# Kernel tuning notes

Hardware: AMD Instinct MI355X
Metric: run time of the kernel (lower is better)

The kernel has to match this reference:

```python
import jax, jax.numpy as jnp
from jax import lax
import numpy as np

SHIFT = 0.0
BN_EPS = 1e-5
THRESHOLD = 0.9
GAMMA = 1.0


def _maxpool2(x):
    # 2x2 max pool, stride 2, NCHW
    return lax.reduce_window(x, -jnp.inf, lax.max, (1, 1, 2, 2), (1, 1, 2, 2), 'VALID')


def _conv(x, w, b):
    y = lax.conv_general_dilated(x, w, (1, 1), 'SAME',
                                 dimension_numbers=('NCHW', 'OIHW', 'NCHW'))
    return y + b[None, :, None, None]


def setup_inputs() -> dict:
    key = jax.random.key(0)
    ks = jax.random.split(key, 12)
    B = 8192
    x = jax.random.normal(ks[0], (B, 1, 28, 28), dtype=jnp.float32)
    conv1_w = jax.random.normal(ks[1], (8, 1, 3, 3), dtype=jnp.float32) * 0.1
    conv1_b = jax.random.normal(ks[2], (8,), dtype=jnp.float32) * 0.1
    conv2_w = jax.random.normal(ks[3], (16, 8, 3, 3), dtype=jnp.float32) * 0.1
    conv2_b = jax.random.normal(ks[4], (16,), dtype=jnp.float32) * 0.1
    fc1_w = jax.random.normal(ks[5], (64, 784), dtype=jnp.float32) * 0.05
    fc1_b = jax.random.normal(ks[6], (64,), dtype=jnp.float32) * 0.05
    fc2_w = jax.random.normal(ks[7], (4, 64), dtype=jnp.float32) * 0.1
    fc2_b = jax.random.normal(ks[8], (4,), dtype=jnp.float32) * 0.1
    bn_gamma = jnp.ones((4,), dtype=jnp.float32)
    bn_beta = jnp.zeros((4,), dtype=jnp.float32)
    return dict(x=x, conv1_w=conv1_w, conv1_b=conv1_b, conv2_w=conv2_w,
                conv2_b=conv2_b, fc1_w=fc1_w, fc1_b=fc1_b, fc2_w=fc2_w,
                fc2_b=fc2_b, bn_gamma=bn_gamma, bn_beta=bn_beta)


def reference(x, conv1_w, conv1_b, conv2_w, conv2_b, fc1_w, fc1_b,
              fc2_w, fc2_b, bn_gamma, bn_beta):
    B = x.shape[0]
    # CNN feature extractor
    h = _maxpool2(jax.nn.relu(_conv(x, conv1_w, conv1_b)))   # [B,8,14,14]
    h = _maxpool2(jax.nn.relu(_conv(h, conv2_w, conv2_b)))   # [B,16,7,7]
    flat = h.reshape(B, -1)                                   # [B,784]
    h = jax.nn.relu(flat @ fc1_w.T + fc1_b)                   # [B,64]
    proj = h @ fc2_w.T + fc2_b                                # [B,4]
    # BatchNorm1d (training mode: batch stats, biased variance)
    mean = jnp.mean(proj, axis=0)
    var = jnp.mean((proj - mean) ** 2, axis=0)
    proj = (proj - mean) * lax.rsqrt(var + BN_EPS) * bn_gamma + bn_beta
    # fidelity adjacency (vectorized O(B^2) pairwise squared cosine overlap)
    pn = proj / (jnp.linalg.norm(proj, axis=1, keepdims=True) + 1e-12)
    fid = (pn @ pn.T) ** 2                                    # [B,B]
    off_diag = 1.0 - jnp.eye(B, dtype=proj.dtype)
    adj = jnp.where(fid >= THRESHOLD, 1.0, 0.0) * off_diag
    adj = lax.stop_gradient(adj)  # built via .item() in torch -> detached
    weighted_proj = adj @ proj                                # [B,4]
    # RBF kernel over the fully-flattened feature matrices (scalar)
    diff = proj - weighted_proj
    k_val = jnp.exp(-GAMMA * jnp.sum(diff * diff))
    # combined.sum(dim=1) == row sums + scalar kernel value
    logits = (jnp.sum(proj, axis=1, keepdims=True)
              + jnp.sum(weighted_proj, axis=1, keepdims=True)
              + k_val)                                        # [B,1]
    probs = jax.nn.sigmoid(logits + SHIFT)
    return jnp.concatenate([probs, 1.0 - probs], axis=-1)     # [B,2]
```

## Files before the change

kernel.cpp:

```cpp
#include <hip/hip_runtime.h>
#include <hip/hip_bf16.h>

#define B_IMG 8192
#define FC_ROWS 8
#define FC_NBLK (B_IMG / FC_ROWS)

#define OFF_SD    64
#define OFF_PROJ  128
#define OFF_PN64  (128 + 262144)
#define OFF_PB32  (OFF_PN64 + 262144)
#define OFF_PN32  (OFF_PB32 + 131072)
#define OFF_WP32  (OFF_PN32 + 131072)
#define OFF_W1T   (OFF_WP32 + 131072)
#define OFF_PSUM  (OFF_W1T + 200704)
#define OFF_FLAT  1310720
#define FLAT64_BYTES (8192UL * 784UL * 8UL)

#define H1_CS   10
#define H1_RP   164

__global__ __launch_bounds__(256) void setup_kernel(
    const float* __restrict__ fc1w, float* __restrict__ w1t,
    float* __restrict__ sd) {
    const int t = threadIdx.x;
    if (blockIdx.x == 0 && t == 0) sd[0] = 0.f;
    for (int i = blockIdx.x * 256 + t; i < 784 * 64; i += 64 * 256) {
        const int o = i & 63, k = i >> 6;
        w1t[i] = fc1w[o * 784 + k];
    }
}

template <int BUF>
__device__ __forceinline__ void ldpair(
    double2 (&W)[2][4][2][2], const double* __restrict__ h1s,
    int rowb, int c0, int icp) {
#pragma unroll
    for (int wr = 0; wr < 4; ++wr) {
#pragma unroll
        for (int cc = 0; cc < 2; ++cc) {
            const double* p = h1s + (rowb + wr) * H1_RP + (c0 + cc) * H1_CS + icp * 4;
            W[BUF][wr][cc][0] = *(const double2*)p;
            W[BUF][wr][cc][1] = *(const double2*)(p + 2);
        }
    }
}

template <int PHASE>
__device__ __forceinline__ void conv2_step(
    const double2 (&W)[2][4][2][2], const double (&wgt)[9][4],
    double bias2, int c2, int icp, int pys, int px,
    double* __restrict__ h2s) {
    double s00 = 0, s01 = 0, s10 = 0, s11 = 0;
#pragma unroll
    for (int dy = 0; dy < 2; ++dy)
#pragma unroll
        for (int dx = 0; dx < 2; ++dx)
#pragma unroll
            for (int ky = 0; ky < 3; ++ky)
#pragma unroll
                for (int kx = 0; kx < 3; ++kx) {
                    const int wr = dy + ky, wc = dx + kx;
                    const int buf = (wc < 2) ? PHASE : (1 - PHASE);
                    const int sl = wc & 1;
                    double2 lo = W[buf][wr][sl][0];
                    double2 hi = W[buf][wr][sl][1];
                    double a = (dy == 0) ? ((dx == 0) ? s00 : s01)
                                         : ((dx == 0) ? s10 : s11);
                    a = fma(lo.x, wgt[ky * 3 + kx][0], a);
                    a = fma(lo.y, wgt[ky * 3 + kx][1], a);
                    a = fma(hi.x, wgt[ky * 3 + kx][2], a);
                    a = fma(hi.y, wgt[ky * 3 + kx][3], a);
                    if (dy == 0) { if (dx == 0) s00 = a; else s01 = a; }
                    else         { if (dx == 0) s10 = a; else s11 = a; }
                }
    s00 += __shfl_xor(s00, 16);
    s01 += __shfl_xor(s01, 16);
    s10 += __shfl_xor(s10, 16);
    s11 += __shfl_xor(s11, 16);
    if (icp == 0) {
        double mx = fmax(fmax(s00, s01), fmax(s10, s11));
        h2s[c2 * 49 + pys * 7 + px] = fmax(bias2 + mx, 0.0);
    }
}

template <bool F64OUT>
__global__ __launch_bounds__(256) void conv_fused(
    const float* __restrict__ x,
    const float* __restrict__ w1, const float* __restrict__ b1,
    const float* __restrict__ w2, const float* __restrict__ b2,
    void* __restrict__ flatv) {

    __shared__ __align__(16) float  xs[900];
    __shared__ __align__(16) double h1s[16 * H1_RP];
    __shared__ __align__(16) double h2s[784];

    const int b = blockIdx.x;
    const int t = threadIdx.x;
    const float* xb = x + (size_t)b * 784;

    const int c2 = t & 15, icp = (t >> 4) & 1, pys = t >> 5;
    double wgt[9][4];
#pragma unroll
    for (int m = 0; m < 4; ++m) {
        const float* wsrc = w2 + c2 * 72 + (icp * 4 + m) * 9;
#pragma unroll
        for (int j = 0; j < 9; ++j) wgt[j][m] = (double)wsrc[j];
    }
    const double bias2 = (double)b2[c2];

    for (int i = t; i < 900; i += 256) xs[i] = 0.f;
    for (int i = t; i < 480; i += 256) {
        const int cell = i >> 3, ic = i & 7;
        int r, c;
        if (cell < 16)      { r = 0;  c = cell; }
        else if (cell < 32) { r = 15; c = cell - 16; }
        else if (cell < 46) { r = cell - 31; c = 0; }
        else                { r = cell - 45; c = 15; }
        h1s[r * H1_RP + c * H1_CS + ic] = 0.0;
    }
    __syncthreads();
    for (int i = t; i < 784; i += 256) {
        const int yy = i / 28, xx = i - yy * 28;
        xs[(yy + 1) * 30 + (xx + 1)] = xb[i];
    }
    __syncthreads();

    {
        const int c1 = t & 7;
        double wc[9];
#pragma unroll
        for (int j = 0; j < 9; ++j) wc[j] = (double)w1[c1 * 9 + j];
        const double bb = (double)b1[c1];
        for (int q = (t >> 3); q < 196; q += 32) {
            const int py = q / 14, px = q - py * 14;
            double r2[4][4];
#pragma unroll
            for (int rr = 0; rr < 4; ++rr)
#pragma unroll
                for (int cc = 0; cc < 4; ++cc)
                    r2[rr][cc] = (double)xs[(2 * py + rr) * 30 + 2 * px + cc];
            double s[2][2] = {{bb, bb}, {bb, bb}};
#pragma unroll
            for (int dy = 0; dy < 2; ++dy)
#pragma unroll
                for (int dx = 0; dx < 2; ++dx)
#pragma unroll
                    for (int ky = 0; ky < 3; ++ky)
#pragma unroll
                        for (int kx = 0; kx < 3; ++kx)
                            s[dy][dx] = fma(r2[dy + ky][dx + kx], wc[ky * 3 + kx], s[dy][dx]);
            double mx = fmax(fmax(s[0][0], s[0][1]), fmax(s[1][0], s[1][1]));
            mx = fmax(mx, 0.0);
            h1s[(py + 1) * H1_RP + (px + 1) * H1_CS + c1] = mx;
        }
    }
    __syncthreads();

    if (pys < 7) {
        const int rowb = 2 * pys;
        double2 W[2][4][2][2];
        ldpair<0>(W, h1s, rowb, 0, icp);
        ldpair<1>(W, h1s, rowb, 2, icp);
#pragma unroll
        for (int px = 0; px < 7; ++px) {
            if ((px & 1) == 0) {
                conv2_step<0>(W, wgt, bias2, c2, icp, pys, px, h2s);
                if (px < 6) ldpair<0>(W, h1s, rowb, 2 * px + 4, icp);
            } else {
                conv2_step<1>(W, wgt, bias2, c2, icp, pys, px, h2s);
                if (px < 6) ldpair<1>(W, h1s, rowb, 2 * px + 4, icp);
            }
        }
    }
    __syncthreads();

    if (F64OUT) {
        double2* dst = (double2*)((double*)flatv + (size_t)b * 784);
        const double2* src = (const double2*)h2s;
        for (int i = t; i < 392; i += 256) dst[i] = src[i];
    } else {
        float* dst = (float*)flatv + (size_t)b * 784;
        for (int i = t; i < 784; i += 256) dst[i] = (float)h2s[i];
    }
}

template <bool F64IN>
__global__ __launch_bounds__(256) void fc_kernel(
    const void* __restrict__ flatv, const float* __restrict__ w1t,
    const float* __restrict__ fc1b,
    const float* __restrict__ fc2w, const float* __restrict__ fc2b,
    double* __restrict__ proj, double* __restrict__ psum) {

    __shared__ __align__(16) double rows[FC_ROWS][784];
    __shared__ __align__(16) double Hs[FC_ROWS][64];
    __shared__ double w2t[256];

    const int t = threadIdx.x;
    const int row0 = blockIdx.x * FC_ROWS;

    w2t[t] = (double)fc2w[(t & 3) * 64 + (t >> 2)];
    if (F64IN) {
        const double2* src = (const double2*)((const double*)flatv + (size_t)row0 * 784);
        double2* dst = (double2*)&rows[0][0];
        for (int i = t; i < FC_ROWS * 784 / 2; i += 256) dst[i] = src[i];
    } else {
        const float4* src = (const float4*)((const float*)flatv + (size_t)row0 * 784);
        double* dst = &rows[0][0];
        for (int i = t; i < FC_ROWS * 784 / 4; i += 256) {
            float4 f = src[i];
            dst[4 * i + 0] = (double)f.x; dst[4 * i + 1] = (double)f.y;
            dst[4 * i + 2] = (double)f.z; dst[4 * i + 3] = (double)f.w;
        }
    }
    __syncthreads();

    const int o = t & 63, s2 = (t >> 6) * 2;
    const double* rp0 = rows[s2];
    const double* rp1 = rows[s2 + 1];
    double a00 = 0.0, a01 = 0.0, a10 = 0.0, a11 = 0.0;
    for (int k = 0; k < 784; k += 4) {
        double2 p0a = *(const double2*)&rp0[k];
        double2 p0b = *(const double2*)&rp0[k + 2];
        double2 p1a = *(const double2*)&rp1[k];
        double2 p1b = *(const double2*)&rp1[k + 2];
        const double wa = (double)w1t[(k + 0) * 64 + o];
        const double wb = (double)w1t[(k + 1) * 64 + o];
        const double wc = (double)w1t[(k + 2) * 64 + o];
        const double wd = (double)w1t[(k + 3) * 64 + o];
        a00 = fma(p0a.x, wa, a00);
        a01 = fma(p0a.y, wb, a01);
        a00 = fma(p0b.x, wc, a00);
        a01 = fma(p0b.y, wd, a01);
        a10 = fma(p1a.x, wa, a10);
        a11 = fma(p1a.y, wb, a11);
        a10 = fma(p1b.x, wc, a10);
        a11 = fma(p1b.y, wd, a11);
    }
    const double b1v = (double)fc1b[o];
    Hs[s2][o]     = fmax((a00 + a01) + b1v, 0.0);
    Hs[s2 + 1][o] = fmax((a10 + a11) + b1v, 0.0);
    __syncthreads();

    if (t < 32) {
        const int r = t >> 2, kc = t & 3;
        double sv = (double)fc2b[kc];
#pragma unroll 8
        for (int c = 0; c < 64; ++c) sv = fma(Hs[r][c], w2t[c * 4 + kc], sv);
        proj[(size_t)(row0 + r) * 4 + kc] = sv;
        double ssum = sv, sq = sv * sv;
        ssum += __shfl_xor(ssum, 4);   sq += __shfl_xor(sq, 4);
        ssum += __shfl_xor(ssum, 8);   sq += __shfl_xor(sq, 8);
        ssum += __shfl_xor(ssum, 16);  sq += __shfl_xor(sq, 16);
        if (t < 4) {
            psum[(size_t)blockIdx.x * 8 + t] = ssum;
            psum[(size_t)blockIdx.x * 8 + 4 + t] = sq;
        }
    }
}

__global__ __launch_bounds__(256) void bn_kernel(
    const double* __restrict__ proj, const double* __restrict__ psum,
    const float* __restrict__ gamma, const float* __restrict__ beta,
    float* __restrict__ pb32, float* __restrict__ pn32,
    double* __restrict__ pn64) {

    __shared__ double red[256];
    __shared__ double stats_s[8];
    const int t = threadIdx.x;
    {
        const int c = t & 7, i0 = t >> 3;
        double v = 0.0;
        for (int i = i0; i < FC_NBLK; i += 32) v += psum[(size_t)i * 8 + c];
        red[t] = v;
    }
    __syncthreads();
    if (t < 8) {
        double sacc = 0.0;
        for (int j = 0; j < 32; ++j) sacc += red[t + 8 * j];
        stats_s[t] = sacc;
    }
    __syncthreads();

    const int i = blockIdx.x * 256 + t;
    double2 p01 = ((const double2*)proj)[2 * i];
    double2 p23 = ((const double2*)proj)[2 * i + 1];
    double pv[4] = {p01.x, p01.y, p23.x, p23.y};
    double o[4];
#pragma unroll
    for (int k = 0; k < 4; ++k) {
        double mean = stats_s[k] * (1.0 / 8192.0);
        double var  = stats_s[4 + k] * (1.0 / 8192.0) - mean * mean;
        double inv  = 1.0 / sqrt(var + 1e-5);
        o[k] = (pv[k] - mean) * inv * (double)gamma[k] + (double)beta[k];
    }
    double nrm = sqrt(o[0] * o[0] + o[1] * o[1] + o[2] * o[2] + o[3] * o[3]);
    double innv = 1.0 / (nrm + 1e-12);
    ((float4*)pb32)[i] = make_float4((float)o[0], (float)o[1], (float)o[2], (float)o[3]);
    double n0 = o[0] * innv, n1 = o[1] * innv, n2 = o[2] * innv, n3 = o[3] * innv;
    ((float4*)pn32)[i] = make_float4((float)n0, (float)n1, (float)n2, (float)n3);
    double2* pd = (double2*)(pn64 + (size_t)i * 4);
    pd[0] = make_double2(n0, n1);
    pd[1] = make_double2(n2, n3);
}

#define CHUNK 1024
__global__ __launch_bounds__(256) void adj_kernel(
    const float* __restrict__ pn32, const float* __restrict__ pb32,
    const double* __restrict__ pn64,
    float* __restrict__ wp32, float* __restrict__ sd) {

    __shared__ __align__(16) float4 pns[CHUNK];
    __shared__ __align__(16) float4 pbs[CHUNK];
    __shared__ float bpart[16];

    const int t = threadIdx.x;
    const int tg = t & 15, g = t >> 4;
    const int row = blockIdx.x * 16 + g;

    const float4 pni = ((const float4*)pn32)[row];
    float w0 = 0.f, w1 = 0.f, w2 = 0.f, w3 = 0.f;

    for (int base = 0; base < 8192; base += CHUNK) {
        for (int i = t; i < CHUNK; i += 256) {
            pns[i] = ((const float4*)pn32)[base + i];
            pbs[i] = ((const float4*)pb32)[base + i];
        }
        __syncthreads();
        for (int jj = 0; jj < CHUNK / 16; ++jj) {
            const int jl = jj * 16 + tg;
            float4 q = pns[jl];
            float4 pj = pbs[jl];
            float d = fmaf(pni.x, q.x, fmaf(pni.y, q.y,
                      fmaf(pni.z, q.z, pni.w * q.w)));
            float fid = d * d;
            float tdiff = fid - 0.9f;
            bool ok;
            if (fabsf(tdiff) < 2e-4f) {
                const int j = base + jl;
                const double2* pr = (const double2*)(pn64 + (size_t)row * 4);
                const double2* pq = (const double2*)(pn64 + (size_t)j * 4);
                double2 r0 = pr[0], r1 = pr[1], q0 = pq[0], q1 = pq[1];
                double dd = fma(r0.x, q0.x, fma(r0.y, q0.y,
                            fma(r1.x, q1.x, r1.y * q1.y)));
                ok = (dd * dd >= 0.9);
            } else {
                ok = (tdiff >= 0.f);
            }
            float m = ok ? 1.f : 0.f;
            w0 = fmaf(m, pj.x, w0);
            w1 = fmaf(m, pj.y, w1);
            w2 = fmaf(m, pj.z, w2);
            w3 = fmaf(m, pj.w, w3);
        }
        __syncthreads();
    }
#pragma unroll
    for (int msk = 1; msk < 16; msk <<= 1) {
        w0 += __shfl_xor(w0, msk);
        w1 += __shfl_xor(w1, msk);
        w2 += __shfl_xor(w2, msk);
        w3 += __shfl_xor(w3, msk);
    }
    if (tg == 0) {
        float4 pbv = ((const float4*)pb32)[row];
        w0 -= pbv.x; w1 -= pbv.y; w2 -= pbv.z; w3 -= pbv.w;
        ((float4*)wp32)[row] = make_float4(w0, w1, w2, w3);
        float d0 = pbv.x - w0, d1 = pbv.y - w1, d2_ = pbv.z - w2, d3 = pbv.w - w3;
        bpart[g] = d0 * d0 + d1 * d1 + d2_ * d2_ + d3 * d3;
    }
    __syncthreads();
    if (t == 0) {
        float sacc = 0.f;
#pragma unroll
        for (int i = 0; i < 16; ++i) sacc += bpart[i];
        atomicAdd(sd, sacc);
    }
}

__global__ __launch_bounds__(256) void final_kernel(
    const float* __restrict__ pb32, const float* __restrict__ wp32,
    const float* __restrict__ sd, float* __restrict__ out) {

    const int i = blockIdx.x * 256 + threadIdx.x;
    const double kv = exp(-(double)sd[0]);
    float4 p = ((const float4*)pb32)[i];
    float4 w = ((const float4*)wp32)[i];
    double logit = (double)p.x + p.y + p.z + p.w
                 + (double)w.x + w.y + w.z + w.w + kv;
    double pr = 1.0 / (1.0 + exp(-logit));
    *(float2*)&out[2 * i] = make_float2((float)pr, (float)(1.0 - pr));
}

extern "C" void kernel_launch(void* const* d_in, const int* in_sizes, int n_in,
                              void* d_out, int out_size, void* d_ws, size_t ws_size,
                              hipStream_t stream) {
    const float* x     = (const float*)d_in[0];
    const float* c1w   = (const float*)d_in[1];
    const float* c1b   = (const float*)d_in[2];
    const float* c2w   = (const float*)d_in[3];
    const float* c2b   = (const float*)d_in[4];
    const float* fc1w  = (const float*)d_in[5];
    const float* fc1b  = (const float*)d_in[6];
    const float* fc2w  = (const float*)d_in[7];
    const float* fc2b  = (const float*)d_in[8];
    const float* gamma = (const float*)d_in[9];
    const float* beta  = (const float*)d_in[10];
    float* out = (float*)d_out;

    char* ws = (char*)d_ws;
    float*  sd    = (float*)(ws + OFF_SD);
    double* proj  = (double*)(ws + OFF_PROJ);
    double* pn64  = (double*)(ws + OFF_PN64);
    float*  pb32  = (float*)(ws + OFF_PB32);
    float*  pn32  = (float*)(ws + OFF_PN32);
    float*  wp32  = (float*)(ws + OFF_WP32);
    float*  w1t   = (float*)(ws + OFF_W1T);
    double* psum  = (double*)(ws + OFF_PSUM);
    void*   flat  = (void*)(ws + OFF_FLAT);

    const bool f64flat = ws_size >= (size_t)OFF_FLAT + FLAT64_BYTES;

    setup_kernel<<<64, 256, 0, stream>>>(fc1w, w1t, sd);
    if (f64flat) {
        conv_fused<true><<<B_IMG, 256, 0, stream>>>(x, c1w, c1b, c2w, c2b, flat);
        fc_kernel<true><<<FC_NBLK, 256, 0, stream>>>(flat, w1t, fc1b, fc2w, fc2b, proj, psum);
    } else {
        conv_fused<false><<<B_IMG, 256, 0, stream>>>(x, c1w, c1b, c2w, c2b, flat);
        fc_kernel<false><<<FC_NBLK, 256, 0, stream>>>(flat, w1t, fc1b, fc2w, fc2b, proj, psum);
    }
    bn_kernel<<<B_IMG / 256, 256, 0, stream>>>(proj, psum, gamma, beta, pb32, pn32, pn64);
    adj_kernel<<<B_IMG / 16, 256, 0, stream>>>(pn32, pb32, pn64, wp32, sd);
    final_kernel<<<B_IMG / 256, 256, 0, stream>>>(pb32, wp32, sd, out);
}
```

Baseline: 357.3 us.

## Register-block adj rows, vectorize fc1 weight loads, pair conv1 outputs

```diff
diff --git a/kernel.cpp b/kernel.cpp
--- a/kernel.cpp
+++ b/kernel.cpp
@@ -26,7 +26,7 @@
     if (blockIdx.x == 0 && t == 0) sd[0] = 0.f;
     for (int i = blockIdx.x * 256 + t; i < 784 * 64; i += 64 * 256) {
         const int o = i & 63, k = i >> 6;
-        w1t[i] = fc1w[o * 784 + k];
+        w1t[(k >> 2) * 256 + o * 4 + (k & 3)] = fc1w[o * 784 + k];
     }
 }
 
@@ -127,19 +127,29 @@
 
     {
         const int c1 = t & 7;
+        const int lq = t >> 3;
         double wc[9];
 #pragma unroll
         for (int j = 0; j < 9; ++j) wc[j] = (double)w1[c1 * 9 + j];
         const double bb = (double)b1[c1];
-        for (int q = (t >> 3); q < 196; q += 32) {
-            const int py = q / 14, px = q - py * 14;
-            double r2[4][4];
+#pragma unroll
+        for (int it = 0; it < 4; ++it) {
+            const int pp = lq + 32 * it;
+            if (pp >= 98) break;
+            const int py = pp / 7, pxp = pp - py * 7;
+            const int px0 = 2 * pxp;
+            const float* xbase = &xs[(2 * py) * 30 + 2 * px0];
+            double dwin[4][6];
 #pragma unroll
             for (int rr = 0; rr < 4; ++rr)
 #pragma unroll
-                for (int cc = 0; cc < 4; ++cc)
-                    r2[rr][cc] = (double)xs[(2 * py + rr) * 30 + 2 * px + cc];
-            double s[2][2] = {{bb, bb}, {bb, bb}};
+                for (int cp = 0; cp < 3; ++cp) {
+                    float2 v = *(const float2*)&xbase[rr * 30 + 2 * cp];
+                    dwin[rr][2 * cp]     = (double)v.x;
+                    dwin[rr][2 * cp + 1] = (double)v.y;
+                }
+            double s0[2][2] = {{bb, bb}, {bb, bb}};
+            double s1[2][2] = {{bb, bb}, {bb, bb}};
 #pragma unroll
             for (int dy = 0; dy < 2; ++dy)
 #pragma unroll
@@ -147,11 +157,17 @@
 #pragma unroll
                     for (int ky = 0; ky < 3; ++ky)
 #pragma unroll
-                        for (int kx = 0; kx < 3; ++kx)
-                            s[dy][dx] = fma(r2[dy + ky][dx + kx], wc[ky * 3 + kx], s[dy][dx]);
-            double mx = fmax(fmax(s[0][0], s[0][1]), fmax(s[1][0], s[1][1]));
-            mx = fmax(mx, 0.0);
-            h1s[(py + 1) * H1_RP + (px + 1) * H1_CS + c1] = mx;
+                        for (int kx = 0; kx < 3; ++kx) {
+                            const double wv = wc[ky * 3 + kx];
+                            s0[dy][dx] = fma(dwin[dy + ky][dx + kx],     wv, s0[dy][dx]);
+                            s1[dy][dx] = fma(dwin[dy + ky][2 + dx + kx], wv, s1[dy][dx]);
+                        }
+            double mx0 = fmax(fmax(s0[0][0], s0[0][1]), fmax(s0[1][0], s0[1][1]));
+            double mx1 = fmax(fmax(s1[0][0], s1[0][1]), fmax(s1[1][0], s1[1][1]));
+            mx0 = fmax(mx0, 0.0);
+            mx1 = fmax(mx1, 0.0);
+            h1s[(py + 1) * H1_RP + (px0 + 1) * H1_CS + c1] = mx0;
+            h1s[(py + 1) * H1_RP + (px0 + 2) * H1_CS + c1] = mx1;
         }
     }
     __syncthreads();
@@ -217,16 +233,16 @@
     const int o = t & 63, s2 = (t >> 6) * 2;
     const double* rp0 = rows[s2];
     const double* rp1 = rows[s2 + 1];
+    const float4* wv4 = (const float4*)w1t;
     double a00 = 0.0, a01 = 0.0, a10 = 0.0, a11 = 0.0;
     for (int k = 0; k < 784; k += 4) {
         double2 p0a = *(const double2*)&rp0[k];
         double2 p0b = *(const double2*)&rp0[k + 2];
         double2 p1a = *(const double2*)&rp1[k];
         double2 p1b = *(const double2*)&rp1[k + 2];
-        const double wa = (double)w1t[(k + 0) * 64 + o];
-        const double wb = (double)w1t[(k + 1) * 64 + o];
-        const double wc = (double)w1t[(k + 2) * 64 + o];
-        const double wd = (double)w1t[(k + 3) * 64 + o];
+        const float4 wv = wv4[(k >> 2) * 64 + o];
+        const double wa = (double)wv.x, wb = (double)wv.y;
+        const double wc = (double)wv.z, wd = (double)wv.w;
         a00 = fma(p0a.x, wa, a00);
         a01 = fma(p0a.y, wb, a01);
         a00 = fma(p0b.x, wc, a00);
@@ -315,10 +331,12 @@
 
     const int t = threadIdx.x;
     const int tg = t & 15, g = t >> 4;
-    const int row = blockIdx.x * 16 + g;
-
-    const float4 pni = ((const float4*)pn32)[row];
-    float w0 = 0.f, w1 = 0.f, w2 = 0.f, w3 = 0.f;
+    const int rowb = blockIdx.x * 32 + g * 2;
+
+    float4 pni[2];
+#pragma unroll
+    for (int r = 0; r < 2; ++r) pni[r] = ((const float4*)pn32)[rowb + r];
+    float w[2][4] = {};
 
     for (int base = 0; base < 8192; base += CHUNK) {
         for (int i = t; i < CHUNK; i += 256) {
@@ -330,43 +348,55 @@
             const int jl = jj * 16 + tg;
             float4 q = pns[jl];
             float4 pj = pbs[jl];
-            float d = fmaf(pni.x, q.x, fmaf(pni.y, q.y,
-                      fmaf(pni.z, q.z, pni.w * q.w)));
-            float fid = d * d;
-            float tdiff = fid - 0.9f;
-            bool ok;
-            if (fabsf(tdiff) < 2e-4f) {
-                const int j = base + jl;
-                const double2* pr = (const double2*)(pn64 + (size_t)row * 4);
-                const double2* pq = (const double2*)(pn64 + (size_t)j * 4);
-                double2 r0 = pr[0], r1 = pr[1], q0 = pq[0], q1 = pq[1];
-                double dd = fma(r0.x, q0.x, fma(r0.y, q0.y,
-                            fma(r1.x, q1.x, r1.y * q1.y)));
-                ok = (dd * dd >= 0.9);
-            } else {
-                ok = (tdiff >= 0.f);
+#pragma unroll
+            for (int r = 0; r < 2; ++r) {
+                float d = fmaf(pni[r].x, q.x, fmaf(pni[r].y, q.y,
+                          fmaf(pni[r].z, q.z, pni[r].w * q.w)));
+                float fid = d * d;
+                float tdiff = fid - 0.9f;
+                bool ok;
+                if (fabsf(tdiff) < 2e-4f) {
+                    const int j = base + jl;
+                    const double2* pr = (const double2*)(pn64 + (size_t)(rowb + r) * 4);
+                    const double2* pq = (const double2*)(pn64 + (size_t)j * 4);
+                    double2 r0 = pr[0], r1 = pr[1], q0 = pq[0], q1 = pq[1];
+                    double dd = fma(r0.x, q0.x, fma(r0.y, q0.y,
+                                fma(r1.x, q1.x, r1.y * q1.y)));
+                    ok = (dd * dd >= 0.9);
+                } else {
+                    ok = (tdiff >= 0.f);
+                }
+                float m = ok ? 1.f : 0.f;
+                w[r][0] = fmaf(m, pj.x, w[r][0]);
+                w[r][1] = fmaf(m, pj.y, w[r][1]);
+                w[r][2] = fmaf(m, pj.z, w[r][2]);
+                w[r][3] = fmaf(m, pj.w, w[r][3]);
             }
-            float m = ok ? 1.f : 0.f;
-            w0 = fmaf(m, pj.x, w0);
-            w1 = fmaf(m, pj.y, w1);
-            w2 = fmaf(m, pj.z, w2);
-            w3 = fmaf(m, pj.w, w3);
         }
         __syncthreads();
     }
 #pragma unroll
-    for (int msk = 1; msk < 16; msk <<= 1) {
-        w0 += __shfl_xor(w0, msk);
-        w1 += __shfl_xor(w1, msk);
-        w2 += __shfl_xor(w2, msk);
-        w3 += __shfl_xor(w3, msk);
-    }
+    for (int msk = 1; msk < 16; msk <<= 1)
+#pragma unroll
+        for (int r = 0; r < 2; ++r) {
+            w[r][0] += __shfl_xor(w[r][0], msk);
+            w[r][1] += __shfl_xor(w[r][1], msk);
+            w[r][2] += __shfl_xor(w[r][2], msk);
+            w[r][3] += __shfl_xor(w[r][3], msk);
+        }
     if (tg == 0) {
-        float4 pbv = ((const float4*)pb32)[row];
-        w0 -= pbv.x; w1 -= pbv.y; w2 -= pbv.z; w3 -= pbv.w;
-        ((float4*)wp32)[row] = make_float4(w0, w1, w2, w3);
-        float d0 = pbv.x - w0, d1 = pbv.y - w1, d2_ = pbv.z - w2, d3 = pbv.w - w3;
-        bpart[g] = d0 * d0 + d1 * d1 + d2_ * d2_ + d3 * d3;
+        float ds_ = 0.f;
+#pragma unroll
+        for (int r = 0; r < 2; ++r) {
+            float4 pbv = ((const float4*)pb32)[rowb + r];
+            float v0 = w[r][0] - pbv.x, v1 = w[r][1] - pbv.y;
+            float v2 = w[r][2] - pbv.z, v3 = w[r][3] - pbv.w;
+            ((float4*)wp32)[rowb + r] = make_float4(v0, v1, v2, v3);
+            float d0 = pbv.x - v0, d1 = pbv.y - v1;
+            float d2 = pbv.z - v2, d3 = pbv.w - v3;
+            ds_ += d0 * d0 + d1 * d1 + d2 * d2 + d3 * d3;
+        }
+        bpart[g] = ds_;
     }
     __syncthreads();
     if (t == 0) {
@@ -429,6 +459,6 @@
         fc_kernel<false><<<FC_NBLK, 256, 0, stream>>>(flat, w1t, fc1b, fc2w, fc2b, proj, psum);
     }
     bn_kernel<<<B_IMG / 256, 256, 0, stream>>>(proj, psum, gamma, beta, pb32, pn32, pn64);
-    adj_kernel<<<B_IMG / 16, 256, 0, stream>>>(pn32, pb32, pn64, wp32, sd);
+    adj_kernel<<<B_IMG / 32, 256, 0, stream>>>(pn32, pb32, pn64, wp32, sd);
     final_kernel<<<B_IMG / 256, 256, 0, stream>>>(pb32, wp32, sd, out);
 }
```

Result: no change. 356.3 us (-0.3%).
